# Kernel tuning notes

Hardware: AMD Instinct MI355X
Metric: run time of the kernel (lower is better)

The kernel has to match this reference:

```python
import jax, jax.numpy as jnp
import numpy as np

B, S, D, H = 4, 1024, 512, 16
HD = D // H
SCALE = 1.0 / np.sqrt(HD).astype(np.float32)


def setup_inputs() -> dict:
    key = jax.random.key(0)
    ks = jax.random.split(key, 20)
    std = 1.0 / np.sqrt(D).astype(np.float32)
    def W(k):
        return jax.random.normal(k, (D, D), jnp.float32) * std
    def b(k):
        return jax.random.normal(k, (D,), jnp.float32) * 0.01
    return {
        "x": jax.random.normal(ks[0], (B, S, D), jnp.float32),
        "ln_g": jnp.ones((D,), jnp.float32),
        "ln_b": jnp.zeros((D,), jnp.float32),
        "Wfa": W(ks[1]), "bfa": b(ks[2]),
        "Whp": W(ks[3]), "bhp": b(ks[4]),
        "Wmg": W(ks[5]), "bmg": b(ks[6]),
        "Wq": W(ks[7]), "bq": b(ks[8]),
        "Wk": W(ks[9]), "bk": b(ks[10]),
        "Wv": W(ks[11]), "bv": b(ks[12]),
        "Wo": W(ks[13]), "bo": b(ks[14]),
    }


def reference(x, ln_g, ln_b, Wfa, bfa, Whp, bhp, Wmg, bmg, Wq, bq, Wk, bk, Wv, bv, Wo, bo):
    residual = x
    # LayerNorm
    mu = jnp.mean(x, axis=-1, keepdims=True)
    var = jnp.mean(jnp.square(x - mu), axis=-1, keepdims=True)
    xn = (x - mu) * jax.lax.rsqrt(var + 1e-5) * ln_g + ln_b

    def lin(h, W, bb):
        return h @ W + bb

    fa = lin(xn, Wfa, bfa).reshape(B, S, H, HD)            # flow anchors, per-head
    hf = lin(xn, Whp, bhp).reshape(B, S, H, HD)            # hierarchical features
    mg = jax.nn.sigmoid(lin(xn, Wmg, bmg)).reshape(B, S, H, HD)  # memory gates
    q = lin(xn, Wq, bq).reshape(B, S, H, HD)
    k = lin(xn, Wk, bk).reshape(B, S, H, HD)
    v = lin(xn, Wv, bv).reshape(B, S, H, HD)

    # anchor weights: softmax over the SEQUENCE axis (dim=1)
    anchor_w = jax.nn.softmax(fa, axis=1)                  # [B,S,H,HD]
    k_weighted = k * anchor_w

    scores = jnp.einsum("bshd,bthd->bsht", q, k_weighted) * SCALE  # [B,S,H,T]
    probs = jax.nn.softmax(scores, axis=2)                 # softmax over HEAD axis (non-standard)
    attn = jnp.einsum("bsht,bthd->bshd", probs, v)         # [B,S,H,HD]

    out = (attn * mg + hf).reshape(B, S, D)
    out = lin(out, Wo, bo)
    return out + residual
```

## Files before the change

### kernel.cpp

```cpp
#include <hip/hip_runtime.h>
#include <hip/hip_bf16.h>
#include <math.h>

#define BB 4
#define SS 1024
#define DD 512
#define HH 16
#define HD 32
#define NTOK (BB * SS)
#define NELEM ((size_t)NTOK * DD)
#define SCALE 0.17677669529663687f
#define SCLOG2E 0.25505526082484745f

typedef __attribute__((ext_vector_type(8))) __bf16 bf16x8;
typedef __attribute__((ext_vector_type(4))) __bf16 bf16x4;
typedef __attribute__((ext_vector_type(4))) float f32x4;
typedef __attribute__((ext_vector_type(4))) unsigned short us4;
typedef __attribute__((ext_vector_type(4))) short s16x4;

__device__ __forceinline__ void gload16(const void* g, void* l) {
    __builtin_amdgcn_global_load_lds(
        (const __attribute__((address_space(1))) void*)g,
        (__attribute__((address_space(3))) void*)l, 16, 0, 0);
}

__global__ __launch_bounds__(256) void ln_kernel(const float* __restrict__ x,
                                                 const float* __restrict__ g,
                                                 const float* __restrict__ bta,
                                                 __bf16* __restrict__ xn) {
    int row = blockIdx.x;
    int tid = threadIdx.x;
    const float* xr = x + (size_t)row * DD;
    float2 v = *reinterpret_cast<const float2*>(&xr[tid * 2]);
    float s1 = v.x + v.y;
    float s2 = v.x * v.x + v.y * v.y;
    for (int off = 32; off > 0; off >>= 1) {
        s1 += __shfl_down(s1, off);
        s2 += __shfl_down(s2, off);
    }
    __shared__ float r1[4], r2[4];
    int w = tid >> 6;
    if ((tid & 63) == 0) { r1[w] = s1; r2[w] = s2; }
    __syncthreads();
    s1 = r1[0] + r1[1] + r1[2] + r1[3];
    s2 = r2[0] + r2[1] + r2[2] + r2[3];
    float mu = s1 * (1.0f / DD);
    float var = s2 * (1.0f / DD) - mu * mu;
    float rstd = rsqrtf(var + 1e-5f);
    float2 gg = *reinterpret_cast<const float2*>(&g[tid * 2]);
    float2 bb = *reinterpret_cast<const float2*>(&bta[tid * 2]);
    __bf16* xp = xn + (size_t)row * DD + tid * 2;
    xp[0] = (__bf16)((v.x - mu) * rstd * gg.x + bb.x);
    xp[1] = (__bf16)((v.y - mu) * rstd * gg.y + bb.y);
}

struct W7 { const float* p[7]; };

__global__ __launch_bounds__(256) void wprep(W7 wp, __bf16* __restrict__ Wt) {
    int z = blockIdx.z;
    int kt = blockIdx.x, nt = blockIdx.y;
    const float* W = wp.p[z];
    __shared__ float lds[32][33];
    int tid = threadIdx.x;
    int r = tid >> 3, c4 = (tid & 7) * 4;
    float4 vv = *reinterpret_cast<const float4*>(W + (size_t)(kt * 32 + r) * DD + nt * 32 + c4);
    lds[r][c4 + 0] = vv.x; lds[r][c4 + 1] = vv.y;
    lds[r][c4 + 2] = vv.z; lds[r][c4 + 3] = vv.w;
    __syncthreads();
    __bf16* o = Wt + (size_t)z * DD * DD + (size_t)(nt * 32 + r) * DD + kt * 32 + c4;
    o[0] = (__bf16)lds[c4 + 0][r];
    o[1] = (__bf16)lds[c4 + 1][r];
    o[2] = (__bf16)lds[c4 + 2][r];
    o[3] = (__bf16)lds[c4 + 3][r];
}

struct GemmCfg { const float* bias[6]; void* out[6]; int mode[6]; };

__global__ __launch_bounds__(256) void mfma_gemm(const __bf16* __restrict__ A,
                                                 const __bf16* __restrict__ Wt0,
                                                 GemmCfg cfg,
                                                 const float* __restrict__ resid) {
    __shared__ __align__(16) char smem[49152];
    int z = blockIdx.z;
    const char* Ab8 = (const char*)A;
    const char* Bb8 = (const char*)(Wt0 + (size_t)z * DD * DD);
    int tid = threadIdx.x;
    int l = tid & 63, wid = tid >> 6;
    int lr = l & 15, lg = l >> 4;
    int wm = wid >> 1, wn = wid & 1;
    int bm = blockIdx.x * 128;
    int bn = blockIdx.y * 64;

    f32x4 acc[4][2];
#pragma unroll
    for (int i = 0; i < 4; ++i)
#pragma unroll
        for (int j = 0; j < 2; ++j) acc[i][j] = (f32x4){0.f, 0.f, 0.f, 0.f};

    auto stage = [&](int k0, int bsel) {
        char* base = smem + bsel * 24576;
#pragma unroll
        for (int i = 0; i < 4; ++i) {
            int r = wid * 32 + i * 8 + (l >> 3);
            int cb = ((l & 7) * 16) ^ ((r & 7) << 4);
            gload16(Ab8 + (size_t)(bm + r) * 1024 + k0 * 2 + cb,
                    base + wid * 4096 + i * 1024);
        }
#pragma unroll
        for (int i = 0; i < 2; ++i) {
            int r = wid * 16 + i * 8 + (l >> 3);
            int cb = ((l & 7) * 16) ^ ((r & 7) << 4);
            gload16(Bb8 + (size_t)(bn + r) * 1024 + k0 * 2 + cb,
                    base + 16384 + wid * 2048 + i * 1024);
        }
    };

    stage(0, 0);
    for (int ks = 0; ks < 8; ++ks) {
        __builtin_amdgcn_s_barrier();
        if (ks < 7) {
            stage((ks + 1) * 64, (ks + 1) & 1);
            asm volatile("s_waitcnt vmcnt(6)" ::: "memory");
        } else {
            asm volatile("s_waitcnt vmcnt(0)" ::: "memory");
        }
        __builtin_amdgcn_s_barrier();
        __builtin_amdgcn_sched_barrier(0);

        const char* cbase = smem + (ks & 1) * 24576;
#pragma unroll
        for (int kk = 0; kk < 2; ++kk) {
            bf16x8 af[4], wf[2];
#pragma unroll
            for (int mi = 0; mi < 4; ++mi) {
                int m = wm * 64 + mi * 16 + lr;
                af[mi] = *reinterpret_cast<const bf16x8*>(
                    cbase + m * 128 + ((kk * 64 + lg * 16) ^ ((m & 7) << 4)));
            }
#pragma unroll
            for (int ni = 0; ni < 2; ++ni) {
                int n = wn * 32 + ni * 16 + lr;
                wf[ni] = *reinterpret_cast<const bf16x8*>(
                    cbase + 16384 + n * 128 + ((kk * 64 + lg * 16) ^ ((n & 7) << 4)));
            }
            __builtin_amdgcn_s_setprio(1);
#pragma unroll
            for (int mi = 0; mi < 4; ++mi)
#pragma unroll
                for (int ni = 0; ni < 2; ++ni)
                    acc[mi][ni] = __builtin_amdgcn_mfma_f32_16x16x32_bf16(af[mi], wf[ni], acc[mi][ni], 0, 0, 0);
            __builtin_amdgcn_s_setprio(0);
        }
    }

    int bmw = bm + wm * 64;
    int bnw = bn + wn * 32;
    int mode = cfg.mode[z];
    const float* bias = cfg.bias[z];
    float bv[2] = {bias[bnw + lr], bias[bnw + 16 + lr]};
#pragma unroll
    for (int mi = 0; mi < 4; ++mi) {
#pragma unroll
        for (int ni = 0; ni < 2; ++ni) {
#pragma unroll
            for (int r = 0; r < 4; ++r) {
                int row = bmw + mi * 16 + lg * 4 + r;
                int col = bnw + ni * 16 + lr;
                float val = acc[mi][ni][r] + bv[ni];
                if (mode == 0) {
                    if (resid) val += resid[(size_t)row * DD + col];
                    ((float*)cfg.out[z])[(size_t)row * DD + col] = val;
                } else if (mode == 1) {
                    val = 1.0f / (1.0f + expf(-val));
                    ((__bf16*)cfg.out[z])[(size_t)row * DD + col] = (__bf16)val;
                } else if (mode == 3) {
                    ((__bf16*)cfg.out[z])[(size_t)row * DD + col] = (__bf16)(val * SCLOG2E);
                } else {
                    ((__bf16*)cfg.out[z])[(size_t)row * DD + col] = (__bf16)val;
                }
            }
        }
    }
}

__global__ __launch_bounds__(256) void anchor_partial(const __bf16* __restrict__ fa,
                                                      float* __restrict__ pmax,
                                                      float* __restrict__ psum) {
    int tx = threadIdx.x;
    int ty = threadIdx.y;
    int c = blockIdx.x * 64 + tx;
    int b = blockIdx.y;
    int sc = blockIdx.z;
    const __bf16* base = fa + ((size_t)(b * SS + sc * 256)) * DD + c;
    float m = -1e30f;
    for (int i = ty; i < 256; i += 4) m = fmaxf(m, (float)base[(size_t)i * DD]);
    __shared__ float red[4][64];
    red[ty][tx] = m;
    __syncthreads();
    float cm = fmaxf(fmaxf(red[0][tx], red[1][tx]), fmaxf(red[2][tx], red[3][tx]));
    float s = 0.f;
    for (int i = ty; i < 256; i += 4) s += expf((float)base[(size_t)i * DD] - cm);
    __syncthreads();
    red[ty][tx] = s;
    __syncthreads();
    if (ty == 0) {
        float tot = red[0][tx] + red[1][tx] + red[2][tx] + red[3][tx];
        int o = (b * 4 + sc) * DD + c;
        pmax[o] = cm;
        psum[o] = tot;
    }
}

__global__ __launch_bounds__(256) void anchor_merge(const float* __restrict__ pmax,
                                                    const float* __restrict__ psum,
                                                    float2* __restrict__ smscale) {
    int idx = blockIdx.x * 256 + threadIdx.x;
    int b = idx >> 9;
    int c = idx & 511;
    float M = -1e30f;
#pragma unroll
    for (int j = 0; j < 4; ++j) M = fmaxf(M, pmax[(b * 4 + j) * DD + c]);
    float Z = 0.f;
#pragma unroll
    for (int j = 0; j < 4; ++j) Z += psum[(b * 4 + j) * DD + c] * expf(pmax[(b * 4 + j) * DD + c] - M);
    smscale[idx] = make_float2(M, 1.0f / Z);
}

__global__ __launch_bounds__(256) void kweight(const __bf16* __restrict__ fa,
                                               const __bf16* __restrict__ kin,
                                               const float2* __restrict__ sm,
                                               __bf16* __restrict__ kw) {
    size_t f = ((size_t)blockIdx.x * 256 + threadIdx.x) * 8;
    int b = (int)(f >> 19);
    int c = (int)(f & 511);
    bf16x8 fv = *reinterpret_cast<const bf16x8*>(fa + f);
    bf16x8 kv = *reinterpret_cast<const bf16x8*>(kin + f);
    const float2* smb = sm + b * DD + c;
    bf16x8 o;
#pragma unroll
    for (int j = 0; j < 8; ++j) {
        float2 s = smb[j];
        o[j] = (__bf16)((float)kv[j] * expf((float)fv[j] - s.x) * s.y);
    }
    *reinterpret_cast<bf16x8*>(kw + f) = o;
}

__global__ __launch_bounds__(256) void vtrans(const __bf16* __restrict__ v,
                                              __bf16* __restrict__ vt) {
    int t0 = blockIdx.x * 32;
    int h = blockIdx.y;
    int b = blockIdx.z;
    __shared__ unsigned short lds[32][33];
    int tid = threadIdx.x;
    int r = tid >> 3, c4 = (tid & 7) * 4;
    const unsigned short* vp = (const unsigned short*)v + ((size_t)(b * SS + t0 + r)) * DD + h * 32 + c4;
    us4 val = *reinterpret_cast<const us4*>(vp);
    lds[r][c4 + 0] = val[0]; lds[r][c4 + 1] = val[1];
    lds[r][c4 + 2] = val[2]; lds[r][c4 + 3] = val[3];
    __syncthreads();
    us4 o;
    o[0] = lds[c4 + 0][r]; o[1] = lds[c4 + 1][r];
    o[2] = lds[c4 + 2][r]; o[3] = lds[c4 + 3][r];
    unsigned short* op = (unsigned short*)vt +
        ((size_t)(b * 128 + ((t0 + c4) >> 3)) * 512 + h * 32 + r) * 8 + (c4 & 7);
    *reinterpret_cast<us4*>(op) = o;
}

struct P4 { __bf16* p[4]; };

__global__ __launch_bounds__(512) void attn_mfma(const __bf16* __restrict__ q,
                                                 const __bf16* __restrict__ kw,
                                                 const __bf16* __restrict__ vt,
                                                 P4 ps) {
    __shared__ __align__(16) char smem[40960];
    int sgq = blockIdx.x;
    int b = blockIdx.y;
    int tp = blockIdx.z;
    int tid = threadIdx.x;
    int wid = tid >> 6;
    int lane = tid & 63;
    int lg = lane >> 4;
    int lr = lane & 15;
    int sgrp = wid & 1;
    int hq = wid >> 1;
    int hbase = hq * 4;
    int s0 = (sgq * 2 + sgrp) * 16;

    const __bf16* qbase = q + ((size_t)(b * SS + s0 + lr)) * DD + lg * 8;
    const char* kwb8 = (const char*)kw + (size_t)b * SS * DD * 2;
    const char* vtb8 = (const char*)vt + (size_t)b * 128 * 8192;

    bf16x8 qf[4];
#pragma unroll
    for (int hi = 0; hi < 4; ++hi)
        qf[hi] = *reinterpret_cast<const bf16x8*>(qbase + (hbase + hi) * 32);

    f32x4 acc[4][2];
#pragma unroll
    for (int hi = 0; hi < 4; ++hi) {
        acc[hi][0] = (f32x4){0.f, 0.f, 0.f, 0.f};
        acc[hi][1] = (f32x4){0.f, 0.f, 0.f, 0.f};
    }

    char* xch = smem + 32768 + (sgrp * 4) * 1024;

    for (int tc = 0; tc < 256; tc += 16) {
        int tbase = tp * 256 + tc;
#pragma unroll
        for (int it = 0; it < 4; ++it) {
            int g = it * 8 + wid;
            if (g < 16) {
                int row = g;
                int colb = (lane * 16) ^ ((row & 15) << 4);
                gload16(kwb8 + (size_t)(tbase + row) * 1024 + colb,
                        smem + row * 1024);
            } else {
                int blkid = g - 16;
                gload16(vtb8 + (size_t)((tbase >> 3) + (blkid >> 3)) * 8192 + (blkid & 7) * 1024 + lane * 16,
                        smem + 16384 + blkid * 1024);
            }
        }
        asm volatile("s_waitcnt vmcnt(0)" ::: "memory");
        __syncthreads();

        f32x4 sc[4];
        bf16x8 ka[4];
#pragma unroll
        for (int hi = 0; hi < 4; ++hi)
            ka[hi] = *reinterpret_cast<const bf16x8*>(
                smem + lr * 1024 + ((((hbase + hi) * 64) + lg * 16) ^ (lr << 4)));
        __builtin_amdgcn_s_setprio(1);
#pragma unroll
        for (int hi = 0; hi < 4; ++hi) {
            f32x4 z = (f32x4){0.f, 0.f, 0.f, 0.f};
            sc[hi] = __builtin_amdgcn_mfma_f32_16x16x32_bf16(ka[hi], qf[hi], z, 0, 0, 0);
        }
        __builtin_amdgcn_s_setprio(0);

#pragma unroll
        for (int hi = 0; hi < 4; ++hi)
#pragma unroll
            for (int r = 0; r < 4; ++r) sc[hi][r] = exp2f(sc[hi][r]);
        f32x4 zsp = sc[0] + sc[1] + sc[2] + sc[3];
        *reinterpret_cast<f32x4*>(xch + hq * 1024 + lane * 16) = zsp;
        __syncthreads();
        f32x4 zt = zsp;
#pragma unroll
        for (int p = 0; p < 4; ++p)
            if (p != hq) zt += *reinterpret_cast<const f32x4*>(xch + p * 1024 + lane * 16);
        float inv[4];
#pragma unroll
        for (int r = 0; r < 4; ++r) inv[r] = __builtin_amdgcn_rcpf(zt[r]);
        bf16x4 pA[4];
#pragma unroll
        for (int hi = 0; hi < 4; ++hi)
#pragma unroll
            for (int r = 0; r < 4; ++r) pA[hi][r] = (__bf16)(sc[hi][r] * inv[r]);

        const char* vb = smem + 16384 + (lg >> 1) * 8192 + (lg & 1) * 8;
#pragma unroll
        for (int hi = 0; hi < 4; hi += 2) {
            s16x4 vf[4];
#pragma unroll
            for (int j = 0; j < 2; ++j) {
                int h = hbase + hi + j;
                vf[2 * j + 0] = *reinterpret_cast<const s16x4*>(vb + (h * 32 + lr) * 16);
                vf[2 * j + 1] = *reinterpret_cast<const s16x4*>(vb + (h * 32 + 16 + lr) * 16);
            }
            __builtin_amdgcn_s_setprio(1);
#pragma unroll
            for (int j = 0; j < 2; ++j) {
                s16x4 pa = __builtin_bit_cast(s16x4, pA[hi + j]);
                acc[hi + j][0] = __builtin_amdgcn_mfma_f32_16x16x16bf16_1k(pa, vf[2 * j + 0], acc[hi + j][0], 0, 0, 0);
                acc[hi + j][1] = __builtin_amdgcn_mfma_f32_16x16x16bf16_1k(pa, vf[2 * j + 1], acc[hi + j][1], 0, 0, 0);
            }
            __builtin_amdgcn_s_setprio(0);
        }
        __syncthreads();
    }

    __bf16* pb = ps.p[tp] + ((size_t)(b * SS + s0)) * DD;
#pragma unroll
    for (int hi = 0; hi < 4; ++hi)
#pragma unroll
        for (int dh = 0; dh < 2; ++dh)
#pragma unroll
            for (int r = 0; r < 4; ++r)
                pb[(size_t)(lg * 4 + r) * DD + (hbase + hi) * 32 + dh * 16 + lr] = (__bf16)acc[hi][dh][r];
}

struct P4c { const __bf16* p[4]; };

__global__ __launch_bounds__(256) void combine_kernel(P4c ps,
                                                      const __bf16* __restrict__ mg,
                                                      const __bf16* __restrict__ hf,
                                                      __bf16* __restrict__ comb) {
    size_t f = ((size_t)blockIdx.x * 256 + threadIdx.x) * 8;
    float accv[8] = {0.f, 0.f, 0.f, 0.f, 0.f, 0.f, 0.f, 0.f};
#pragma unroll
    for (int i = 0; i < 4; ++i) {
        bf16x8 v = *reinterpret_cast<const bf16x8*>(ps.p[i] + f);
#pragma unroll
        for (int j = 0; j < 8; ++j) accv[j] += (float)v[j];
    }
    bf16x8 m = *reinterpret_cast<const bf16x8*>(mg + f);
    bf16x8 hh = *reinterpret_cast<const bf16x8*>(hf + f);
    bf16x8 o;
#pragma unroll
    for (int j = 0; j < 8; ++j) o[j] = (__bf16)(accv[j] * (float)m[j] + (float)hh[j]);
    *reinterpret_cast<bf16x8*>(comb + f) = o;
}

extern "C" void kernel_launch(void* const* d_in, const int* in_sizes, int n_in,
                              void* d_out, int out_size, void* d_ws, size_t ws_size,
                              hipStream_t stream) {
    const float* x    = (const float*)d_in[0];
    const float* ln_g = (const float*)d_in[1];
    const float* ln_b = (const float*)d_in[2];
    const float* Wfa  = (const float*)d_in[3];  const float* bfa = (const float*)d_in[4];
    const float* Whp  = (const float*)d_in[5];  const float* bhp = (const float*)d_in[6];
    const float* Wmg  = (const float*)d_in[7];  const float* bmg = (const float*)d_in[8];
    const float* Wq   = (const float*)d_in[9];  const float* bq  = (const float*)d_in[10];
    const float* Wk   = (const float*)d_in[11]; const float* bk  = (const float*)d_in[12];
    const float* Wv   = (const float*)d_in[13]; const float* bv  = (const float*)d_in[14];
    const float* Wo   = (const float*)d_in[15]; const float* bo  = (const float*)d_in[16];
    float* out = (float*)d_out;

    char* w8 = (char*)d_ws;
    __bf16* Wt   = (__bf16*)(w8 + ((size_t) 0 << 20));
    __bf16* xn   = (__bf16*)(w8 + ((size_t) 4 << 20));
    __bf16* fa   = (__bf16*)(w8 + ((size_t) 8 << 20));
    __bf16* hf   = (__bf16*)(w8 + ((size_t)12 << 20));
    __bf16* mg   = (__bf16*)(w8 + ((size_t)16 << 20));
    __bf16* q    = (__bf16*)(w8 + ((size_t)20 << 20));
    __bf16* k    = (__bf16*)(w8 + ((size_t)24 << 20));
    __bf16* v    = (__bf16*)(w8 + ((size_t)28 << 20));
    __bf16* kw   = (__bf16*)(w8 + ((size_t)32 << 20));
    __bf16* vt   = (__bf16*)(w8 + ((size_t)36 << 20));
    P4 ps;
    ps.p[0] = (__bf16*)(w8 + ((size_t) 4 << 20));
    ps.p[1] = (__bf16*)(w8 + ((size_t) 8 << 20));
    ps.p[2] = (__bf16*)(w8 + ((size_t)24 << 20));
    ps.p[3] = (__bf16*)(w8 + ((size_t)28 << 20));
    __bf16* comb = (__bf16*)(w8 + ((size_t)56 << 20));
    float* pmax  = (float*) (w8 + ((size_t)60 << 20));
    float* psum  = pmax + 16 * DD;
    float2* smsc = (float2*)(psum + 16 * DD);

    ln_kernel<<<NTOK, 256, 0, stream>>>(x, ln_g, ln_b, xn);

    W7 wp; wp.p[0]=Wfa; wp.p[1]=Whp; wp.p[2]=Wmg; wp.p[3]=Wq; wp.p[4]=Wk; wp.p[5]=Wv; wp.p[6]=Wo;
    wprep<<<dim3(16, 16, 7), 256, 0, stream>>>(wp, Wt);

    GemmCfg cfg;
    cfg.bias[0]=bfa; cfg.out[0]=fa; cfg.mode[0]=2;
    cfg.bias[1]=bhp; cfg.out[1]=hf; cfg.mode[1]=2;
    cfg.bias[2]=bmg; cfg.out[2]=mg; cfg.mode[2]=1;
    cfg.bias[3]=bq;  cfg.out[3]=q;  cfg.mode[3]=3;
    cfg.bias[4]=bk;  cfg.out[4]=k;  cfg.mode[4]=2;
    cfg.bias[5]=bv;  cfg.out[5]=v;  cfg.mode[5]=2;
    mfma_gemm<<<dim3(32, 8, 6), 256, 0, stream>>>(xn, Wt, cfg, nullptr);

    anchor_partial<<<dim3(8, 4, 4), dim3(64, 4), 0, stream>>>(fa, pmax, psum);
    anchor_merge<<<8, 256, 0, stream>>>(pmax, psum, smsc);
    kweight<<<1024, 256, 0, stream>>>(fa, k, smsc, kw);

    vtrans<<<dim3(32, 16, 4), 256, 0, stream>>>(v, vt);

    attn_mfma<<<dim3(32, 4, 4), 512, 0, stream>>>(q, kw, vt, ps);

    P4c pc;
    for (int i = 0; i < 4; ++i) pc.p[i] = ps.p[i];
    combine_kernel<<<1024, 256, 0, stream>>>(pc, mg, hf, comb);

    GemmCfg cfg2;
    for (int i = 0; i < 6; ++i) { cfg2.bias[i]=bo; cfg2.out[i]=out; cfg2.mode[i]=0; }
    mfma_gemm<<<dim3(32, 8, 1), 256, 0, stream>>>(comb, Wt + (size_t)6 * DD * DD, cfg2, x);
}
```

Baseline: 133.9 us.

## Double-buffer K/V LDS tiles in attention kernel to overlap loads with compute

Moves the attention kernel to two LDS buffers for the weighted-K and transposed-V tiles and prefetches the next chunk with async global-to-LDS loads while the current chunk is processed. Waits become partial vmcnt waits with split barriers, so K readiness and V readiness are checked separately. The softmax-exchange scratch now reuses the current K buffer after the score MFMAs finish. The goal is to hide global load latency behind the score, exp and PV work. The cost is more LDS (64KB, which can reduce occupancy) and more barriers per iteration.

```diff
diff --git a/kernel.cpp b/kernel.cpp
--- a/kernel.cpp
+++ b/kernel.cpp
@@ -272,7 +272,7 @@
                                                  const __bf16* __restrict__ kw,
                                                  const __bf16* __restrict__ vt,
                                                  P4 ps) {
-    __shared__ __align__(16) char smem[40960];
+    __shared__ __align__(16) char smem[65536];
     int sgq = blockIdx.x;
     int b = blockIdx.y;
     int tp = blockIdx.z;
@@ -302,33 +302,41 @@
         acc[hi][1] = (f32x4){0.f, 0.f, 0.f, 0.f};
     }
 
-    char* xch = smem + 32768 + (sgrp * 4) * 1024;
+    auto stage = [&](int tbase, int bsel) {
+#pragma unroll
+        for (int i = 0; i < 2; ++i) {
+            int row = wid + i * 8;
+            int colb = (lane * 16) ^ ((row & 15) << 4);
+            gload16(kwb8 + (size_t)(tbase + row) * 1024 + colb,
+                    smem + bsel * 16384 + row * 1024);
+        }
+#pragma unroll
+        for (int i = 0; i < 2; ++i) {
+            int blkid = wid + i * 8;
+            gload16(vtb8 + (size_t)((tbase >> 3) + (blkid >> 3)) * 8192 + (blkid & 7) * 1024 + lane * 16,
+                    smem + 32768 + bsel * 16384 + blkid * 1024);
+        }
+    };
+
+    int tbase0 = tp * 256;
+    stage(tbase0, 0);
 
     for (int tc = 0; tc < 256; tc += 16) {
-        int tbase = tp * 256 + tc;
-#pragma unroll
-        for (int it = 0; it < 4; ++it) {
-            int g = it * 8 + wid;
-            if (g < 16) {
-                int row = g;
-                int colb = (lane * 16) ^ ((row & 15) << 4);
-                gload16(kwb8 + (size_t)(tbase + row) * 1024 + colb,
-                        smem + row * 1024);
-            } else {
-                int blkid = g - 16;
-                gload16(vtb8 + (size_t)((tbase >> 3) + (blkid >> 3)) * 8192 + (blkid & 7) * 1024 + lane * 16,
-                        smem + 16384 + blkid * 1024);
-            }
-        }
-        asm volatile("s_waitcnt vmcnt(0)" ::: "memory");
-        __syncthreads();
+        int cur = (tc >> 4) & 1;
+        char* kwbuf = smem + cur * 16384;
+        char* vtbuf = smem + 32768 + cur * 16384;
+        char* xch = kwbuf + sgrp * 4096;
+
+        asm volatile("s_waitcnt vmcnt(2)" ::: "memory");
+        __builtin_amdgcn_s_barrier();
+        __builtin_amdgcn_sched_barrier(0);
 
         f32x4 sc[4];
         bf16x8 ka[4];
 #pragma unroll
         for (int hi = 0; hi < 4; ++hi)
             ka[hi] = *reinterpret_cast<const bf16x8*>(
-                smem + lr * 1024 + ((((hbase + hi) * 64) + lg * 16) ^ (lr << 4)));
+                kwbuf + lr * 1024 + ((((hbase + hi) * 64) + lg * 16) ^ (lr << 4)));
         __builtin_amdgcn_s_setprio(1);
 #pragma unroll
         for (int hi = 0; hi < 4; ++hi) {
@@ -337,13 +345,20 @@
         }
         __builtin_amdgcn_s_setprio(0);
 
+        __builtin_amdgcn_s_barrier();
+        __builtin_amdgcn_sched_barrier(0);
+
 #pragma unroll
         for (int hi = 0; hi < 4; ++hi)
 #pragma unroll
             for (int r = 0; r < 4; ++r) sc[hi][r] = exp2f(sc[hi][r]);
         f32x4 zsp = sc[0] + sc[1] + sc[2] + sc[3];
         *reinterpret_cast<f32x4*>(xch + hq * 1024 + lane * 16) = zsp;
-        __syncthreads();
+        if (tc + 16 < 256) stage(tbase0 + tc + 16, cur ^ 1);
+        asm volatile("s_waitcnt lgkmcnt(0)" ::: "memory");
+        __builtin_amdgcn_s_barrier();
+        __builtin_amdgcn_sched_barrier(0);
+
         f32x4 zt = zsp;
 #pragma unroll
         for (int p = 0; p < 4; ++p)
@@ -357,7 +372,15 @@
 #pragma unroll
             for (int r = 0; r < 4; ++r) pA[hi][r] = (__bf16)(sc[hi][r] * inv[r]);
 
-        const char* vb = smem + 16384 + (lg >> 1) * 8192 + (lg & 1) * 8;
+        if (tc + 16 < 256) {
+            asm volatile("s_waitcnt vmcnt(4)" ::: "memory");
+        } else {
+            asm volatile("s_waitcnt vmcnt(0)" ::: "memory");
+        }
+        __builtin_amdgcn_s_barrier();
+        __builtin_amdgcn_sched_barrier(0);
+
+        const char* vb = vtbuf + (lg >> 1) * 8192 + (lg & 1) * 8;
 #pragma unroll
         for (int hi = 0; hi < 4; hi += 2) {
             s16x4 vf[4];
@@ -376,7 +399,6 @@
             }
             __builtin_amdgcn_s_setprio(0);
         }
-        __syncthreads();
     }
 
     __bf16* pb = ps.p[tp] + ((size_t)(b * SS + s0)) * DD;
```

Result: no change. 132.9 us (-0.7%).
